# Optimization experiments

Measured on AMD Instinct MI355X. Metric: run time of the kernel, lower is better.

The kernel has to match this reference:

```python
import jax, jax.numpy as jnp
import numpy as np

FIXED_POINT = 4
LOGMAX = 7
MAX_INT8 = 127
B, H = 16384, 2048


def _clipped_add(*ts):
    r = ts[0].astype(jnp.int32)
    for t in ts[1:]:
        r = r + t.astype(jnp.int32)
    return jnp.clip(r, -MAX_INT8, MAX_INT8).astype(jnp.int8)


def _int_matmul(x, w):
    # x: (..., in) int8, w: (out, in) int8 -> (..., out) int8
    r = jnp.matmul(x.astype(jnp.int32), w.T.astype(jnp.int32))
    scale = (2 ** FIXED_POINT) * int(np.sqrt(w.shape[-1]))  # 16 * 45 = 720 for H=2048
    r = r // scale  # floor division, matches torch // on ints
    return jnp.clip(r, -MAX_INT8, MAX_INT8).astype(jnp.int8)


def setup_inputs() -> dict:
    key = jax.random.key(0)
    k_x, k_s, k_wf, k_uf, k_wh, k_uh = jax.random.split(key, 6)

    def init_w(k):
        w = jax.random.normal(k, (H, H), dtype=jnp.float32) * (2 ** FIXED_POINT)
        return jnp.clip(jnp.round(w), -MAX_INT8, MAX_INT8).astype(jnp.int8)

    x = jax.random.randint(k_x, (B, H), -MAX_INT8, MAX_INT8 + 1, dtype=jnp.int32).astype(jnp.int8)
    state = jax.random.randint(k_s, (B, H), -MAX_INT8, MAX_INT8 + 1, dtype=jnp.int32).astype(jnp.int8)
    return {
        "x": x,
        "state": state,
        "W_f": init_w(k_wf),
        "U_f": init_w(k_uf),
        "b_f": jnp.zeros((H,), dtype=jnp.int8),
        "W_h": init_w(k_wh),
        "U_h": init_w(k_uh),
        "b_h": jnp.zeros((H,), dtype=jnp.int8),
    }


def reference(x, state, W_f, U_f, b_f, W_h, U_h, b_h):
    f_t = _clipped_add(_int_matmul(x, W_f), _int_matmul(state, U_f), b_f)
    f_gate = f_t.astype(jnp.int32) + MAX_INT8  # in [0, 254]
    # note: torch `a >> LOGMAX + 1` parses as a >> (LOGMAX + 1) == >> 8 (arithmetic shift)
    gated_past = (f_gate * state.astype(jnp.int32)) >> (LOGMAX + 1)
    gated_past = jnp.clip(gated_past, -MAX_INT8, MAX_INT8).astype(jnp.int8)
    h_tilde = _clipped_add(_int_matmul(x, W_h), _int_matmul(gated_past, U_h), b_h)
    diff = h_tilde.astype(jnp.int32) - state.astype(jnp.int32)
    new_state = state.astype(jnp.int32) + ((f_gate * diff) >> (LOGMAX + 1))
    new_state = jnp.clip(new_state, -MAX_INT8, MAX_INT8).astype(jnp.int8)
    return (new_state, new_state)
```

## Files before the change

kernel.cpp:

```cpp
#include <hip/hip_runtime.h>
#include <stdint.h>

#define HH 2048
#define BB 16384

typedef int v4i __attribute__((ext_vector_type(4)));

__device__ __forceinline__ int clip127(int v){
  v = v > 127 ? 127 : v;
  return v < -127 ? -127 : v;
}
__device__ __forceinline__ int fdiv720(int r){
  int q = r / 720;
  return q - ((r - q * 720) < 0 ? 1 : 0);
}

__global__ void pack_i32_to_i8(const int* __restrict__ src, int8_t* __restrict__ dst, int n16){
  int stride = gridDim.x * blockDim.x;
  for (int i = blockIdx.x * blockDim.x + threadIdx.x; i < n16; i += stride){
    const int4* s = (const int4*)src + (size_t)i * 4;
    int4 a = s[0], b = s[1], c = s[2], d = s[3];
    int4 o;
    o.x = (a.x & 255) | ((a.y & 255) << 8) | ((a.z & 255) << 16) | (a.w << 24);
    o.y = (b.x & 255) | ((b.y & 255) << 8) | ((b.z & 255) << 16) | (b.w << 24);
    o.z = (c.x & 255) | ((c.y & 255) << 8) | ((c.z & 255) << 16) | (c.w << 24);
    o.w = (d.x & 255) | ((d.y & 255) << 8) | ((d.z & 255) << 16) | (d.w << 24);
    ((int4*)dst)[i] = o;
  }
}

__global__ void dup_out(const int* __restrict__ src, int* __restrict__ dst, int n4){
  int stride = gridDim.x * blockDim.x;
  for (int i = blockIdx.x * blockDim.x + threadIdx.x; i < n4; i += stride)
    ((int4*)dst)[i] = ((const int4*)src)[i];
}

template<int PHASE>
__global__ __launch_bounds__(256, 2)
void gemm_fused(const int8_t* __restrict__ A1, const int8_t* __restrict__ A2,
                const int8_t* __restrict__ B1, const int8_t* __restrict__ B2,
                const int* __restrict__ bias,
                const int8_t* __restrict__ state8,
                int* fbuf,
                int8_t* __restrict__ g8out)
{
  __shared__ __align__(16) int8_t lds[4 * 8192];
  const int tid  = threadIdx.x;
  const int lane = tid & 63;
  const int wave = tid >> 6;
  const int wrow = wave >> 1, wcol = wave & 1;
  const int bid  = blockIdx.x;
  const int rowbase = (bid >> 4) * 128;
  const int colbase = (bid & 15) * 128;

  v4i accA[4][4], accB[4][4];
  const v4i vzero = {0, 0, 0, 0};
#pragma unroll
  for (int m = 0; m < 4; m++)
#pragma unroll
    for (int n = 0; n < 4; n++){ accA[m][n] = vzero; accB[m][n] = vzero; }

  const int srow   = tid >> 2;
  const int schunk = tid & 3;
  const int chunk  = lane >> 4;
  const int rl     = lane & 15;

  for (int kk = 0; kk < HH / 64; ++kk){
    const int k0 = kk * 64;
#pragma unroll
    for (int p = 0; p < 2; p++){
      const int row = p * 64 + srow;
      const int swc = schunk ^ ((row >> 1) & 3);
      const size_t aoff = (size_t)(rowbase + row) * HH + k0 + swc * 16;
      const size_t boff = (size_t)(colbase + row) * HH + k0 + swc * 16;
      const int ldst = p * 4096 + tid * 16;
      __builtin_amdgcn_global_load_lds((const __attribute__((address_space(1))) void*)(A1 + aoff),
                                       (__attribute__((address_space(3))) void*)(lds + ldst), 16, 0, 0);
      __builtin_amdgcn_global_load_lds((const __attribute__((address_space(1))) void*)(A2 + aoff),
                                       (__attribute__((address_space(3))) void*)(lds + 8192 + ldst), 16, 0, 0);
      __builtin_amdgcn_global_load_lds((const __attribute__((address_space(1))) void*)(B1 + boff),
                                       (__attribute__((address_space(3))) void*)(lds + 16384 + ldst), 16, 0, 0);
      __builtin_amdgcn_global_load_lds((const __attribute__((address_space(1))) void*)(B2 + boff),
                                       (__attribute__((address_space(3))) void*)(lds + 24576 + ldst), 16, 0, 0);
    }
    __syncthreads();

    {
      v4i af[4], bf[4];
#pragma unroll
      for (int m = 0; m < 4; m++){
        int row = wrow * 64 + m * 16 + rl;
        af[m] = *(const v4i*)(lds + row * 64 + ((chunk ^ ((row >> 1) & 3)) << 4));
      }
#pragma unroll
      for (int n = 0; n < 4; n++){
        int row = wcol * 64 + n * 16 + rl;
        bf[n] = *(const v4i*)(lds + 16384 + row * 64 + ((chunk ^ ((row >> 1) & 3)) << 4));
      }
#pragma unroll
      for (int m = 0; m < 4; m++)
#pragma unroll
        for (int n = 0; n < 4; n++)
          accA[m][n] = __builtin_amdgcn_mfma_i32_16x16x64_i8(af[m], bf[n], accA[m][n], 0, 0, 0);
    }
    {
      v4i af[4], bf[4];
#pragma unroll
      for (int m = 0; m < 4; m++){
        int row = wrow * 64 + m * 16 + rl;
        af[m] = *(const v4i*)(lds + 8192 + row * 64 + ((chunk ^ ((row >> 1) & 3)) << 4));
      }
#pragma unroll
      for (int n = 0; n < 4; n++){
        int row = wcol * 64 + n * 16 + rl;
        bf[n] = *(const v4i*)(lds + 24576 + row * 64 + ((chunk ^ ((row >> 1) & 3)) << 4));
      }
#pragma unroll
      for (int m = 0; m < 4; m++)
#pragma unroll
        for (int n = 0; n < 4; n++)
          accB[m][n] = __builtin_amdgcn_mfma_i32_16x16x64_i8(af[m], bf[n], accB[m][n], 0, 0, 0);
    }
    __syncthreads();
  }

  const int q = lane >> 4;
#pragma unroll
  for (int m = 0; m < 4; m++){
#pragma unroll
    for (int n = 0; n < 4; n++){
      const int gcol = colbase + wcol * 64 + n * 16 + rl;
      const int bval = bias[gcol];
#pragma unroll
      for (int r = 0; r < 4; r++){
        const int grow = rowbase + wrow * 64 + m * 16 + q * 4 + r;
        const size_t idx = (size_t)grow * HH + gcol;
        const int v1 = clip127(fdiv720(accA[m][n][r]));
        const int v2 = clip127(fdiv720(accB[m][n][r]));
        const int t  = clip127(v1 + v2 + bval);
        const int st = state8[idx];
        if (PHASE == 1){
          const int fg = t + 127;
          const int gated = clip127((fg * st) >> 8);
          fbuf[idx]  = fg;
          g8out[idx] = (int8_t)gated;
        } else {
          const int fg   = fbuf[idx];
          const int diff = t - st;
          const int ns   = clip127(st + ((fg * diff) >> 8));
          fbuf[idx] = ns;
        }
      }
    }
  }
}

extern "C" void kernel_launch(void* const* d_in, const int* in_sizes, int n_in,
                              void* d_out, int out_size, void* d_ws, size_t ws_size,
                              hipStream_t stream){
  const int* x  = (const int*)d_in[0];
  const int* st = (const int*)d_in[1];
  const int* Wf = (const int*)d_in[2];
  const int* Uf = (const int*)d_in[3];
  const int* bf = (const int*)d_in[4];
  const int* Wh = (const int*)d_in[5];
  const int* Uh = (const int*)d_in[6];
  const int* bh = (const int*)d_in[7];

  const size_t NBH = (size_t)BB * HH;
  const size_t NW  = (size_t)HH * HH;

  int*    fbuf = (int*)d_out;
  int8_t* base = (int8_t*)d_out + (size_t)NBH * 4;
  int8_t* x8  = base;
  int8_t* s8  = x8 + NBH;
  int8_t* g8  = s8 + NBH;
  int8_t* wf8 = g8 + NBH;
  int8_t* uf8 = wf8 + NW;
  int8_t* wh8 = uf8 + NW;
  int8_t* uh8 = wh8 + NW;

  pack_i32_to_i8<<<2048, 256, 0, stream>>>(x,  x8,  (int)(NBH / 16));
  pack_i32_to_i8<<<2048, 256, 0, stream>>>(st, s8,  (int)(NBH / 16));
  pack_i32_to_i8<<<1024, 256, 0, stream>>>(Wf, wf8, (int)(NW / 16));
  pack_i32_to_i8<<<1024, 256, 0, stream>>>(Uf, uf8, (int)(NW / 16));
  pack_i32_to_i8<<<1024, 256, 0, stream>>>(Wh, wh8, (int)(NW / 16));
  pack_i32_to_i8<<<1024, 256, 0, stream>>>(Uh, uh8, (int)(NW / 16));

  gemm_fused<1><<<2048, 256, 0, stream>>>(x8, s8, wf8, uf8, bf, s8, fbuf, g8);
  gemm_fused<2><<<2048, 256, 0, stream>>>(x8, g8, wh8, uh8, bh, s8, fbuf, nullptr);

  dup_out<<<2048, 256, 0, stream>>>((const int*)d_out,
                                    (int*)d_out + NBH, (int)(NBH / 4));
}
```

Measured before the change: 566.8 us.

## Split fused dual GEMMs into four 256x256 double-buffered GEMM passes

Replaces the two dual-operand GEMM kernels with four single-operand GEMMs using 256x256 tiles, 512 threads, BK=128 and double-buffered LDS prefetch via global_load_lds. Each GEMM's partial result goes to an intermediate buffer (int32 or int8), and the gates are combined in the epilogue of later passes. The block index is remapped so that consecutive blocks share the same weight tile, for L2 reuse. In exchange the kernel makes extra intermediate global reads and writes, uses 128KB of LDS per block, and the larger accumulator may raise register pressure.

Measured after the change: 631.8 us. 1.11x slower.

```diff
diff --git a/kernel.cpp b/kernel.cpp
--- a/kernel.cpp
+++ b/kernel.cpp
@@ -3,6 +3,8 @@
 
 #define HH 2048
 #define BB 16384
+#define BK 128
+#define NK (HH / BK)
 
 typedef int v4i __attribute__((ext_vector_type(4)));
 
@@ -35,120 +37,112 @@
     ((int4*)dst)[i] = ((const int4*)src)[i];
 }
 
-template<int PHASE>
-__global__ __launch_bounds__(256, 2)
-void gemm_fused(const int8_t* __restrict__ A1, const int8_t* __restrict__ A2,
-                const int8_t* __restrict__ B1, const int8_t* __restrict__ B2,
-                const int* __restrict__ bias,
-                const int8_t* __restrict__ state8,
-                int* fbuf,
-                int8_t* __restrict__ g8out)
+template<int E>
+__global__ __launch_bounds__(512, 2)
+void gemm256(const int8_t* __restrict__ A, const int8_t* __restrict__ B,
+             const int* __restrict__ bias, const int8_t* __restrict__ s8,
+             int8_t* io8, uint8_t* fg8, int* out1)
 {
-  __shared__ __align__(16) int8_t lds[4 * 8192];
+  __shared__ __align__(16) int8_t lds[2 * 65536];
   const int tid  = threadIdx.x;
   const int lane = tid & 63;
   const int wave = tid >> 6;
-  const int wrow = wave >> 1, wcol = wave & 1;
-  const int bid  = blockIdx.x;
-  const int rowbase = (bid >> 4) * 128;
-  const int colbase = (bid & 15) * 128;
+  const int wr   = wave >> 2;
+  const int wc   = wave & 3;
 
-  v4i accA[4][4], accB[4][4];
-  const v4i vzero = {0, 0, 0, 0};
+  const int bid = blockIdx.x;
+  const int wg  = (bid & 7) * 64 + (bid >> 3);
+  const int rowbase = (wg >> 3) * 256;
+  const int colbase = (wg & 7) * 256;
+
+  const int srow = tid >> 3;
+  const int sc   = tid & 7;
+  const int rl   = lane & 15;
+  const int ch   = lane >> 4;
+
+  v4i acc[8][4];
+  const v4i vz = {0,0,0,0};
 #pragma unroll
-  for (int m = 0; m < 4; m++)
+  for (int m = 0; m < 8; m++)
 #pragma unroll
-    for (int n = 0; n < 4; n++){ accA[m][n] = vzero; accB[m][n] = vzero; }
+    for (int n = 0; n < 4; n++) acc[m][n] = vz;
 
-  const int srow   = tid >> 2;
-  const int schunk = tid & 3;
-  const int chunk  = lane >> 4;
-  const int rl     = lane & 15;
+  auto STAGE = [&](int buf, int kk){
+    const int k0 = kk * BK;
+    const int base = buf * 65536;
+#pragma unroll
+    for (int p = 0; p < 4; p++){
+      const int row = p * 64 + srow;
+      const int scx = sc ^ (row & 7);
+      __builtin_amdgcn_global_load_lds(
+        (const __attribute__((address_space(1))) void*)(A + (size_t)(rowbase + row) * HH + k0 + scx * 16),
+        (__attribute__((address_space(3))) void*)(lds + base + p * 8192 + tid * 16), 16, 0, 0);
+      __builtin_amdgcn_global_load_lds(
+        (const __attribute__((address_space(1))) void*)(B + (size_t)(colbase + row) * HH + k0 + scx * 16),
+        (__attribute__((address_space(3))) void*)(lds + base + 32768 + p * 8192 + tid * 16), 16, 0, 0);
+    }
+  };
 
-  for (int kk = 0; kk < HH / 64; ++kk){
-    const int k0 = kk * 64;
+  int cur = 0;
+  STAGE(0, 0);
+  __syncthreads();
+
+  for (int kk = 0; kk < NK; ++kk){
+    if (kk + 1 < NK) STAGE(cur ^ 1, kk + 1);
+    const int cb = cur * 65536;
 #pragma unroll
-    for (int p = 0; p < 2; p++){
-      const int row = p * 64 + srow;
-      const int swc = schunk ^ ((row >> 1) & 3);
-      const size_t aoff = (size_t)(rowbase + row) * HH + k0 + swc * 16;
-      const size_t boff = (size_t)(colbase + row) * HH + k0 + swc * 16;
-      const int ldst = p * 4096 + tid * 16;
-      __builtin_amdgcn_global_load_lds((const __attribute__((address_space(1))) void*)(A1 + aoff),
-                                       (__attribute__((address_space(3))) void*)(lds + ldst), 16, 0, 0);
-      __builtin_amdgcn_global_load_lds((const __attribute__((address_space(1))) void*)(A2 + aoff),
-                                       (__attribute__((address_space(3))) void*)(lds + 8192 + ldst), 16, 0, 0);
-      __builtin_amdgcn_global_load_lds((const __attribute__((address_space(1))) void*)(B1 + boff),
-                                       (__attribute__((address_space(3))) void*)(lds + 16384 + ldst), 16, 0, 0);
-      __builtin_amdgcn_global_load_lds((const __attribute__((address_space(1))) void*)(B2 + boff),
-                                       (__attribute__((address_space(3))) void*)(lds + 24576 + ldst), 16, 0, 0);
-    }
-    __syncthreads();
-
-    {
-      v4i af[4], bf[4];
+    for (int k2 = 0; k2 < 2; ++k2){
+      v4i af[8], bf[4];
 #pragma unroll
-      for (int m = 0; m < 4; m++){
-        int row = wrow * 64 + m * 16 + rl;
-        af[m] = *(const v4i*)(lds + row * 64 + ((chunk ^ ((row >> 1) & 3)) << 4));
+      for (int m = 0; m < 8; m++){
+        const int row = wr * 128 + m * 16 + rl;
+        const int c = (k2 * 4 + ch) ^ (row & 7);
+        af[m] = *(const v4i*)(lds + cb + row * BK + c * 16);
       }
 #pragma unroll
       for (int n = 0; n < 4; n++){
-        int row = wcol * 64 + n * 16 + rl;
-        bf[n] = *(const v4i*)(lds + 16384 + row * 64 + ((chunk ^ ((row >> 1) & 3)) << 4));
+        const int row = wc * 64 + n * 16 + rl;
+        const int c = (k2 * 4 + ch) ^ (row & 7);
+        bf[n] = *(const v4i*)(lds + cb + 32768 + row * BK + c * 16);
       }
 #pragma unroll
-      for (int m = 0; m < 4; m++)
+      for (int m = 0; m < 8; m++)
 #pragma unroll
         for (int n = 0; n < 4; n++)
-          accA[m][n] = __builtin_amdgcn_mfma_i32_16x16x64_i8(af[m], bf[n], accA[m][n], 0, 0, 0);
-    }
-    {
-      v4i af[4], bf[4];
-#pragma unroll
-      for (int m = 0; m < 4; m++){
-        int row = wrow * 64 + m * 16 + rl;
-        af[m] = *(const v4i*)(lds + 8192 + row * 64 + ((chunk ^ ((row >> 1) & 3)) << 4));
-      }
-#pragma unroll
-      for (int n = 0; n < 4; n++){
-        int row = wcol * 64 + n * 16 + rl;
-        bf[n] = *(const v4i*)(lds + 24576 + row * 64 + ((chunk ^ ((row >> 1) & 3)) << 4));
-      }
-#pragma unroll
-      for (int m = 0; m < 4; m++)
-#pragma unroll
-        for (int n = 0; n < 4; n++)
-          accB[m][n] = __builtin_amdgcn_mfma_i32_16x16x64_i8(af[m], bf[n], accB[m][n], 0, 0, 0);
+          acc[m][n] = __builtin_amdgcn_mfma_i32_16x16x64_i8(af[m], bf[n], acc[m][n], 0, 0, 0);
     }
     __syncthreads();
+    cur ^= 1;
   }
 
   const int q = lane >> 4;
 #pragma unroll
-  for (int m = 0; m < 4; m++){
+  for (int m = 0; m < 8; m++){
 #pragma unroll
     for (int n = 0; n < 4; n++){
-      const int gcol = colbase + wcol * 64 + n * 16 + rl;
-      const int bval = bias[gcol];
+      const int gcol = colbase + wc * 64 + n * 16 + rl;
 #pragma unroll
       for (int r = 0; r < 4; r++){
-        const int grow = rowbase + wrow * 64 + m * 16 + q * 4 + r;
+        const int grow = rowbase + wr * 128 + m * 16 + q * 4 + r;
         const size_t idx = (size_t)grow * HH + gcol;
-        const int v1 = clip127(fdiv720(accA[m][n][r]));
-        const int v2 = clip127(fdiv720(accB[m][n][r]));
-        const int t  = clip127(v1 + v2 + bval);
-        const int st = state8[idx];
-        if (PHASE == 1){
-          const int fg = t + 127;
-          const int gated = clip127((fg * st) >> 8);
-          fbuf[idx]  = fg;
-          g8out[idx] = (int8_t)gated;
+        const int v2 = clip127(fdiv720(acc[m][n][r]));
+        if (E == 0){
+          out1[idx] = v2;
+        } else if (E == 1){
+          io8[idx] = (int8_t)v2;
+        } else if (E == 2){
+          const int v1 = io8[idx];
+          const int ft = clip127(v1 + v2 + bias[gcol]);
+          const int fg = ft + 127;
+          const int st = s8[idx];
+          io8[idx] = (int8_t)clip127((fg * st) >> 8);
+          fg8[idx] = (uint8_t)fg;
         } else {
-          const int fg   = fbuf[idx];
-          const int diff = t - st;
-          const int ns   = clip127(st + ((fg * diff) >> 8));
-          fbuf[idx] = ns;
+          const int v3 = out1[idx];
+          const int h  = clip127(v3 + v2 + bias[gcol]);
+          const int st = s8[idx];
+          const int fg = (int)fg8[idx];
+          out1[idx] = clip127(st + ((fg * (h - st)) >> 8));
         }
       }
     }
@@ -170,26 +164,27 @@
   const size_t NBH = (size_t)BB * HH;
   const size_t NW  = (size_t)HH * HH;
 
-  int*    fbuf = (int*)d_out;
-  int8_t* base = (int8_t*)d_out + (size_t)NBH * 4;
-  int8_t* x8  = base;
-  int8_t* s8  = x8 + NBH;
-  int8_t* g8  = s8 + NBH;
-  int8_t* wf8 = g8 + NBH;
-  int8_t* uf8 = wf8 + NW;
-  int8_t* wh8 = uf8 + NW;
-  int8_t* uh8 = wh8 + NW;
+  int*    out1 = (int*)d_out;
+  int8_t* b2   = (int8_t*)d_out + (size_t)NBH * 4;
+  int8_t* s8   = b2;
+  int8_t* P    = b2 + NBH;
+  int8_t* F    = b2 + 2 * NBH;
+  int8_t* wh8  = b2 + 3 * NBH;
+  int8_t* wf8  = wh8 + NW;
+  int8_t* uf8  = wf8 + NW;
+  int8_t* uh8  = uf8 + NW;
 
-  pack_i32_to_i8<<<2048, 256, 0, stream>>>(x,  x8,  (int)(NBH / 16));
+  pack_i32_to_i8<<<2048, 256, 0, stream>>>(x,  F,   (int)(NBH / 16));
   pack_i32_to_i8<<<2048, 256, 0, stream>>>(st, s8,  (int)(NBH / 16));
+  pack_i32_to_i8<<<1024, 256, 0, stream>>>(Wh, wh8, (int)(NW / 16));
   pack_i32_to_i8<<<1024, 256, 0, stream>>>(Wf, wf8, (int)(NW / 16));
   pack_i32_to_i8<<<1024, 256, 0, stream>>>(Uf, uf8, (int)(NW / 16));
-  pack_i32_to_i8<<<1024, 256, 0, stream>>>(Wh, wh8, (int)(NW / 16));
   pack_i32_to_i8<<<1024, 256, 0, stream>>>(Uh, uh8, (int)(NW / 16));
 
-  gemm_fused<1><<<2048, 256, 0, stream>>>(x8, s8, wf8, uf8, bf, s8, fbuf, g8);
-  gemm_fused<2><<<2048, 256, 0, stream>>>(x8, g8, wh8, uh8, bh, s8, fbuf, nullptr);
+  gemm256<0><<<512, 512, 0, stream>>>(F,  wh8, nullptr, nullptr, nullptr, nullptr, out1);
+  gemm256<1><<<512, 512, 0, stream>>>(F,  wf8, nullptr, nullptr, P,       nullptr, nullptr);
+  gemm256<2><<<512, 512, 0, stream>>>(s8, uf8, bf,      s8,      P,       (uint8_t*)F, nullptr);
+  gemm256<3><<<512, 512, 0, stream>>>(P,  uh8, bh,      s8,      nullptr, (uint8_t*)F, out1);
 
-  dup_out<<<2048, 256, 0, stream>>>((const int*)d_out,
-                                    (int*)d_out + NBH, (int)(NBH / 4));
+  dup_out<<<2048, 256, 0, stream>>>(out1, out1 + NBH, (int)(NBH / 4));
 }
```

## Double-buffer LDS tiles, swizzle block order, and write second output in epilogue

Applied to the files above, without the earlier changes.

Doubles the LDS buffer so the next K-slice loads via global_load_lds while MFMAs run on the current one, cutting one barrier per iteration. It remaps block indices so consecutive workgroups share weight columns, which should improve L2 reuse. When the workspace is large enough, the packed int8 buffers move there and phase 2 writes both outputs directly, skipping the separate copy kernel. The cost is double the LDS (64KB per block), which may limit occupancy at 2 blocks per CU.

Result: slower. 621.8 us (+9.7%).

```diff
diff --git a/kernel.cpp b/kernel.cpp
--- a/kernel.cpp
+++ b/kernel.cpp
@@ -3,6 +3,7 @@
 
 #define HH 2048
 #define BB 16384
+#define NK (HH / 64)
 
 typedef int v4i __attribute__((ext_vector_type(4)));
 
@@ -37,21 +38,22 @@
 
 template<int PHASE>
 __global__ __launch_bounds__(256, 2)
-void gemm_fused(const int8_t* __restrict__ A1, const int8_t* __restrict__ A2,
-                const int8_t* __restrict__ B1, const int8_t* __restrict__ B2,
-                const int* __restrict__ bias,
-                const int8_t* __restrict__ state8,
-                int* fbuf,
-                int8_t* __restrict__ g8out)
+void gemm_dual(const int8_t* __restrict__ A1, const int8_t* __restrict__ A2,
+               const int8_t* __restrict__ B1, const int8_t* __restrict__ B2,
+               const int* __restrict__ bias,
+               const int8_t* __restrict__ state8,
+               int* fbuf, int8_t* __restrict__ g8out, int* __restrict__ out2)
 {
-  __shared__ __align__(16) int8_t lds[4 * 8192];
+  __shared__ __align__(16) int8_t lds[2 * 32768];
   const int tid  = threadIdx.x;
   const int lane = tid & 63;
   const int wave = tid >> 6;
   const int wrow = wave >> 1, wcol = wave & 1;
-  const int bid  = blockIdx.x;
-  const int rowbase = (bid >> 4) * 128;
-  const int colbase = (bid & 15) * 128;
+
+  const int bid = blockIdx.x;
+  const int wg  = (bid & 7) * 256 + (bid >> 3);
+  const int rowbase = (wg >> 4) * 128;
+  const int colbase = (wg & 15) * 128;
 
   v4i accA[4][4], accB[4][4];
   const v4i vzero = {0, 0, 0, 0};
@@ -65,15 +67,16 @@
   const int chunk  = lane >> 4;
   const int rl     = lane & 15;
 
-  for (int kk = 0; kk < HH / 64; ++kk){
+  auto STAGE = [&](int buf, int kk){
     const int k0 = kk * 64;
+    const int bb = buf * 32768;
 #pragma unroll
     for (int p = 0; p < 2; p++){
       const int row = p * 64 + srow;
       const int swc = schunk ^ ((row >> 1) & 3);
       const size_t aoff = (size_t)(rowbase + row) * HH + k0 + swc * 16;
       const size_t boff = (size_t)(colbase + row) * HH + k0 + swc * 16;
-      const int ldst = p * 4096 + tid * 16;
+      const int ldst = bb + p * 4096 + tid * 16;
       __builtin_amdgcn_global_load_lds((const __attribute__((address_space(1))) void*)(A1 + aoff),
                                        (__attribute__((address_space(3))) void*)(lds + ldst), 16, 0, 0);
       __builtin_amdgcn_global_load_lds((const __attribute__((address_space(1))) void*)(A2 + aoff),
@@ -83,19 +86,26 @@
       __builtin_amdgcn_global_load_lds((const __attribute__((address_space(1))) void*)(B2 + boff),
                                        (__attribute__((address_space(3))) void*)(lds + 24576 + ldst), 16, 0, 0);
     }
-    __syncthreads();
-
+  };
+
+  int cur = 0;
+  STAGE(0, 0);
+  __syncthreads();
+
+  for (int kk = 0; kk < NK; ++kk){
+    if (kk + 1 < NK) STAGE(cur ^ 1, kk + 1);
+    const int cb = cur * 32768;
     {
       v4i af[4], bf[4];
 #pragma unroll
       for (int m = 0; m < 4; m++){
-        int row = wrow * 64 + m * 16 + rl;
-        af[m] = *(const v4i*)(lds + row * 64 + ((chunk ^ ((row >> 1) & 3)) << 4));
+        const int row = wrow * 64 + m * 16 + rl;
+        af[m] = *(const v4i*)(lds + cb + row * 64 + ((chunk ^ ((row >> 1) & 3)) << 4));
       }
 #pragma unroll
       for (int n = 0; n < 4; n++){
-        int row = wcol * 64 + n * 16 + rl;
-        bf[n] = *(const v4i*)(lds + 16384 + row * 64 + ((chunk ^ ((row >> 1) & 3)) << 4));
+        const int row = wcol * 64 + n * 16 + rl;
+        bf[n] = *(const v4i*)(lds + cb + 16384 + row * 64 + ((chunk ^ ((row >> 1) & 3)) << 4));
       }
 #pragma unroll
       for (int m = 0; m < 4; m++)
@@ -107,13 +117,13 @@
       v4i af[4], bf[4];
 #pragma unroll
       for (int m = 0; m < 4; m++){
-        int row = wrow * 64 + m * 16 + rl;
-        af[m] = *(const v4i*)(lds + 8192 + row * 64 + ((chunk ^ ((row >> 1) & 3)) << 4));
+        const int row = wrow * 64 + m * 16 + rl;
+        af[m] = *(const v4i*)(lds + cb + 8192 + row * 64 + ((chunk ^ ((row >> 1) & 3)) << 4));
       }
 #pragma unroll
       for (int n = 0; n < 4; n++){
-        int row = wcol * 64 + n * 16 + rl;
-        bf[n] = *(const v4i*)(lds + 24576 + row * 64 + ((chunk ^ ((row >> 1) & 3)) << 4));
+        const int row = wcol * 64 + n * 16 + rl;
+        bf[n] = *(const v4i*)(lds + cb + 24576 + row * 64 + ((chunk ^ ((row >> 1) & 3)) << 4));
       }
 #pragma unroll
       for (int m = 0; m < 4; m++)
@@ -122,6 +132,7 @@
           accB[m][n] = __builtin_amdgcn_mfma_i32_16x16x64_i8(af[m], bf[n], accB[m][n], 0, 0, 0);
     }
     __syncthreads();
+    cur ^= 1;
   }
 
   const int q = lane >> 4;
@@ -141,14 +152,13 @@
         const int st = state8[idx];
         if (PHASE == 1){
           const int fg = t + 127;
-          const int gated = clip127((fg * st) >> 8);
           fbuf[idx]  = fg;
-          g8out[idx] = (int8_t)gated;
+          g8out[idx] = (int8_t)clip127((fg * st) >> 8);
         } else {
-          const int fg   = fbuf[idx];
-          const int diff = t - st;
-          const int ns   = clip127(st + ((fg * diff) >> 8));
+          const int fg = fbuf[idx];
+          const int ns = clip127(st + ((fg * (t - st)) >> 8));
           fbuf[idx] = ns;
+          if (out2) out2[idx] = ns;
         }
       }
     }
@@ -169,9 +179,11 @@
 
   const size_t NBH = (size_t)BB * HH;
   const size_t NW  = (size_t)HH * HH;
-
-  int*    fbuf = (int*)d_out;
-  int8_t* base = (int8_t*)d_out + (size_t)NBH * 4;
+  const size_t need = 3 * NBH + 4 * NW;
+
+  int*    out1   = (int*)d_out;
+  const bool wsp = (ws_size >= need);
+  int8_t* base   = wsp ? (int8_t*)d_ws : (int8_t*)d_out + NBH * 4;
   int8_t* x8  = base;
   int8_t* s8  = x8 + NBH;
   int8_t* g8  = s8 + NBH;
@@ -187,9 +199,10 @@
   pack_i32_to_i8<<<1024, 256, 0, stream>>>(Wh, wh8, (int)(NW / 16));
   pack_i32_to_i8<<<1024, 256, 0, stream>>>(Uh, uh8, (int)(NW / 16));
 
-  gemm_fused<1><<<2048, 256, 0, stream>>>(x8, s8, wf8, uf8, bf, s8, fbuf, g8);
-  gemm_fused<2><<<2048, 256, 0, stream>>>(x8, g8, wh8, uh8, bh, s8, fbuf, nullptr);
-
-  dup_out<<<2048, 256, 0, stream>>>((const int*)d_out,
-                                    (int*)d_out + NBH, (int)(NBH / 4));
-}
+  gemm_dual<1><<<2048, 256, 0, stream>>>(x8, s8, wf8, uf8, bf, s8, out1, g8, nullptr);
+  gemm_dual<2><<<2048, 256, 0, stream>>>(x8, g8, wh8, uh8, bh, s8, out1, nullptr,
+                                         wsp ? out1 + NBH : nullptr);
+
+  if (!wsp)
+    dup_out<<<2048, 256, 0, stream>>>(out1, out1 + NBH, (int)(NBH / 4));
+}
```
